# Kernel tuning notes

Measured on AMD Instinct MI355X. Metric: run time of the kernel, lower is better.

Reference implementation:

```python
import jax, jax.numpy as jnp
import numpy as np

L, D, H, F = 6, 768, 12, 3072   # layers, d_model, heads, mlp hidden
B, S = 2, 2048                   # batch, seq_len
DH = D // H                      # head dim
EPS = 1e-5


def _layer_norm(x, w, b):
    mu = jnp.mean(x, axis=-1, keepdims=True)
    var = jnp.mean(jnp.square(x - mu), axis=-1, keepdims=True)
    return (x - mu) * jax.lax.rsqrt(var + EPS) * w + b


def setup_inputs() -> dict:
    key = jax.random.key(0)
    ks = jax.random.split(key, 8)
    w = lambda k, shape: jax.random.normal(k, shape, dtype=jnp.float32) * 0.02
    return {
        "x": jax.random.normal(ks[0], (B, S, D), dtype=jnp.float32),
        # attention projections, stacked over layers; weights stored (d_in, d_out)
        "Wq": w(ks[1], (L, D, D)), "bq": jnp.zeros((L, D), jnp.float32),
        "Wk": w(ks[2], (L, D, D)), "bk": jnp.zeros((L, D), jnp.float32),
        "Wv": w(ks[3], (L, D, D)), "bv": jnp.zeros((L, D), jnp.float32),
        "Wo": w(ks[4], (L, D, D)), "bo": jnp.zeros((L, D), jnp.float32),
        "ln1_w": jnp.ones((L, D), jnp.float32), "ln1_b": jnp.zeros((L, D), jnp.float32),
        "W1": w(ks[5], (L, D, F)), "b1": jnp.zeros((L, F), jnp.float32),
        "W2": w(ks[6], (L, F, D)), "b2": jnp.zeros((L, D), jnp.float32),
        "ln2_w": jnp.ones((L, D), jnp.float32), "ln2_b": jnp.zeros((L, D), jnp.float32),
        "lnf_w": jnp.ones((D,), jnp.float32), "lnf_b": jnp.zeros((D,), jnp.float32),
    }


def reference(x, Wq, bq, Wk, bk, Wv, bv, Wo, bo, ln1_w, ln1_b,
              W1, b1, W2, b2, ln2_w, ln2_b, lnf_w, lnf_b):
    scale = DH ** (-0.5)
    for i in range(L):
        # pre-norm MSA block; NB: residual uses the normalized x, as in source
        xn = _layer_norm(x, ln1_w[i], ln1_b[i])
        q = (xn @ Wq[i] + bq[i]).reshape(B, S, H, DH).transpose(0, 2, 1, 3)
        k = (xn @ Wk[i] + bk[i]).reshape(B, S, H, DH).transpose(0, 2, 1, 3)
        v = (xn @ Wv[i] + bv[i]).reshape(B, S, H, DH).transpose(0, 2, 1, 3)
        att = jax.nn.softmax(scale * jnp.einsum('bhqd,bhkd->bhqk', q, k), axis=-1)
        out = jnp.einsum('bhqk,bhkd->bhqd', att, v)
        out = out.transpose(0, 2, 1, 3).reshape(B, S, D)
        x = xn + (out @ Wo[i] + bo[i])
        # pre-norm FFN block; residual uses the normalized x, as in source
        xn2 = _layer_norm(x, ln2_w[i], ln2_b[i])
        h = jax.nn.gelu(xn2 @ W1[i] + b1[i], approximate=False)
        x = xn2 + (h @ W2[i] + b2[i])
    return _layer_norm(x, lnf_w, lnf_b)
```

## Files before the change

### kernel.cpp

```cpp
#include <hip/hip_runtime.h>
#include <stdint.h>

typedef unsigned short u16;
typedef unsigned int   u32;

#define L_N  6
#define D_N  768
#define F_N  3072
#define H_N  12
#define B_N  2
#define S_N  2048
#define BS_N 4096
#define QKV_N 2304
#define CSC  0.18033688011112042f
#define DTHR 11.54f

using bf16x8 = __attribute__((ext_vector_type(8))) short;
using f32x4  = __attribute__((ext_vector_type(4))) float;
using f32x16 = __attribute__((ext_vector_type(16))) float;
using u32x2  = __attribute__((ext_vector_type(2))) unsigned int;

__device__ __forceinline__ u16 f2bf(float f) {
  u32 x = __builtin_bit_cast(u32, f);
  x += 0x7FFFu + ((x >> 16) & 1u);
  return (u16)(x >> 16);
}

__device__ __forceinline__ float bf2f(u16 v) {
  return __builtin_bit_cast(float, (u32)v << 16);
}

__device__ __forceinline__ u32 cvt_pk_bf16(float lo, float hi) {
  u32 r;
  asm("v_cvt_pk_bf16_f32 %0, %1, %2" : "=v"(r) : "v"(lo), "v"(hi));
  return r;
}

#define GLOAD16(g, l)                                                                     \
  __builtin_amdgcn_global_load_lds((const __attribute__((address_space(1))) void*)(g),    \
                                   (__attribute__((address_space(3))) void*)(l), 16, 0, 0)

__global__ __launch_bounds__(256) void transpose_cast_kernel(
    const float* __restrict__ in, u16* __restrict__ out, int K, int N,
    size_t out_lstride, int out_rowoff)
{
  __shared__ float tile[32][33];
  const int l  = blockIdx.z;
  const int n0 = blockIdx.x * 32, k0 = blockIdx.y * 32;
  const int tx = threadIdx.x & 31, ty = threadIdx.x >> 5;
  const float* src = in + (size_t)l * K * N;
  u16* dst = out + (size_t)l * out_lstride + (size_t)out_rowoff * K;
#pragma unroll
  for (int i = 0; i < 4; ++i)
    tile[ty + i * 8][tx] = src[(size_t)(k0 + ty + i * 8) * N + n0 + tx];
  __syncthreads();
#pragma unroll
  for (int i = 0; i < 4; ++i)
    dst[(size_t)(n0 + ty + i * 8) * K + k0 + tx] = f2bf(tile[tx][ty + i * 8]);
}

__global__ __launch_bounds__(256) void concat_bias_kernel(
    const float* __restrict__ bq, const float* __restrict__ bk,
    const float* __restrict__ bv, float* __restrict__ out)
{
  const int i = blockIdx.x * 256 + threadIdx.x;
  const int l = i / QKV_N, c = i - l * QKV_N;
  float v = (c < 768) ? bq[l * 768 + c]
          : (c < 1536) ? bk[l * 768 + c - 768]
                       : bv[l * 768 + c - 1536];
  out[i] = v;
}

template<bool BF16IN>
__global__ __launch_bounds__(256) void ln_kernel(
    const void* __restrict__ xv, const float* __restrict__ w, const float* __restrict__ b,
    float* __restrict__ outF, u16* __restrict__ outB)
{
  const int row = blockIdx.x, tid = threadIdx.x;
  float v[3];
  float s = 0.f;
  if (BF16IN) {
    const u16* xr = (const u16*)xv + (size_t)row * D_N;
#pragma unroll
    for (int i = 0; i < 3; ++i) { v[i] = bf2f(xr[tid + i * 256]); s += v[i]; }
  } else {
    const float* xr = (const float*)xv + (size_t)row * D_N;
#pragma unroll
    for (int i = 0; i < 3; ++i) { v[i] = xr[tid + i * 256]; s += v[i]; }
  }
  __shared__ float red[8];
  const int wave = tid >> 6, lane = tid & 63;
#pragma unroll
  for (int o = 32; o > 0; o >>= 1) s += __shfl_down(s, o, 64);
  if (lane == 0) red[wave] = s;
  __syncthreads();
  const float mu = (red[0] + red[1] + red[2] + red[3]) * (1.f / D_N);
  float d2 = 0.f;
#pragma unroll
  for (int i = 0; i < 3; ++i) { float d = v[i] - mu; d2 += d * d; }
#pragma unroll
  for (int o = 32; o > 0; o >>= 1) d2 += __shfl_down(d2, o, 64);
  if (lane == 0) red[4 + wave] = d2;
  __syncthreads();
  const float var = (red[4] + red[5] + red[6] + red[7]) * (1.f / D_N);
  const float rs = rsqrtf(var + 1e-5f);
#pragma unroll
  for (int i = 0; i < 3; ++i) {
    const int c = tid + i * 256;
    const float o = (v[i] - mu) * rs * w[c] + b[c];
    if (outF) outF[(size_t)row * D_N + c] = o;
    if (outB) outB[(size_t)row * D_N + c] = f2bf(o);
  }
}

template<bool GELU, bool OUTB, bool SCALEQ>
__global__ __launch_bounds__(256) void gemm_kernel(
    const u16* __restrict__ A, const u16* __restrict__ Wt,
    const float* __restrict__ bias,
    u16* __restrict__ outB, int M, int N, int K)
{
  __shared__ __align__(16) u16 As[2][128 * 32];
  __shared__ __align__(16) u16 Bs[2][128 * 32];
  const int tid  = threadIdx.x;
  const int wave = tid >> 6, lane = tid & 63;
  const int lr = lane & 15, lg = lane >> 4;
  const int row0 = blockIdx.x * 128, col0 = blockIdx.y * 128;
  const int wr = (wave >> 1) * 64, wc = (wave & 1) * 64;

  const int cb0 = wave * 64;
  const int cb1 = 256 + wave * 64;
  const int r0s = (cb0 + lane) >> 2, c0s = ((cb0 + lane) & 3) << 3;
  const int r1s = (cb1 + lane) >> 2, c1s = ((cb1 + lane) & 3) << 3;

  f32x4 acc[4][4] = {};

#define STAGE(cbuf, kk)                                                           \
  do {                                                                            \
    GLOAD16(A  + (size_t)(row0 + r0s) * K + (kk) + c0s, &As[cbuf][cb0 * 8]);      \
    GLOAD16(Wt + (size_t)(col0 + r0s) * K + (kk) + c0s, &Bs[cbuf][cb0 * 8]);      \
    GLOAD16(A  + (size_t)(row0 + r1s) * K + (kk) + c1s, &As[cbuf][cb1 * 8]);      \
    GLOAD16(Wt + (size_t)(col0 + r1s) * K + (kk) + c1s, &Bs[cbuf][cb1 * 8]);      \
  } while (0)

  STAGE(0, 0);
  __syncthreads();

  int c = 0;
  for (int k0 = 0; k0 < K; k0 += 32, c ^= 1) {
    if (k0 + 32 < K) STAGE(c ^ 1, k0 + 32);
    bf16x8 af[4], bfr[4];
#pragma unroll
    for (int m = 0; m < 4; ++m)
      af[m] = *(const bf16x8*)&As[c][(wr + m * 16 + lr) * 32 + lg * 8];
#pragma unroll
    for (int n = 0; n < 4; ++n)
      bfr[n] = *(const bf16x8*)&Bs[c][(wc + n * 16 + lr) * 32 + lg * 8];
    __builtin_amdgcn_s_setprio(1);
#pragma unroll
    for (int m = 0; m < 4; ++m)
#pragma unroll
      for (int n = 0; n < 4; ++n)
        acc[m][n] = __builtin_amdgcn_mfma_f32_16x16x32_bf16(af[m], bfr[n], acc[m][n], 0, 0, 0);
    __builtin_amdgcn_s_setprio(0);
    __syncthreads();
  }
#undef STAGE

#pragma unroll
  for (int m = 0; m < 4; ++m)
#pragma unroll
    for (int n = 0; n < 4; ++n) {
      const int col = col0 + wc + n * 16 + lr;
      const float bv = bias[col];
#pragma unroll
      for (int r = 0; r < 4; ++r) {
        const int row = row0 + wr + m * 16 + lg * 4 + r;
        float v = acc[m][n][r] + bv;
        if (GELU) v = 0.5f * v * (1.f + erff(v * 0.70710678118f));
        if (SCALEQ && col < 768) v *= CSC;
        const size_t idx = (size_t)row * N + col;
        if (OUTB) outB[idx] = f2bf(v);
      }
    }
}

__global__ __launch_bounds__(256) void gemm64_kernel(
    const u16* __restrict__ A, const u16* __restrict__ Wt,
    const float* __restrict__ bias, const u16* __restrict__ resid,
    u16* __restrict__ outB, int M, int N, int K)
{
  __shared__ __align__(16) u16 As[2][64 * 32];
  __shared__ __align__(16) u16 Bs[2][64 * 32];
  const int tid  = threadIdx.x;
  const int wave = tid >> 6, lane = tid & 63;
  const int lr = lane & 15, lg = lane >> 4;
  const int row0 = blockIdx.x * 64, col0 = blockIdx.y * 64;
  const int wr = (wave >> 1) * 32, wc = (wave & 1) * 32;

  const int cb = wave * 64;
  const int ch = cb + lane;
  const int rs = ch >> 2, cs = (ch & 3) << 3;

  f32x4 acc[2][2] = {};

#define STAGE64(cbuf, kk)                                                         \
  do {                                                                            \
    GLOAD16(A  + (size_t)(row0 + rs) * K + (kk) + cs, &As[cbuf][cb * 8]);         \
    GLOAD16(Wt + (size_t)(col0 + rs) * K + (kk) + cs, &Bs[cbuf][cb * 8]);         \
  } while (0)

  STAGE64(0, 0);
  __syncthreads();

  int c = 0;
  for (int k0 = 0; k0 < K; k0 += 32, c ^= 1) {
    if (k0 + 32 < K) STAGE64(c ^ 1, k0 + 32);
    bf16x8 af[2], bfr[2];
#pragma unroll
    for (int m = 0; m < 2; ++m)
      af[m] = *(const bf16x8*)&As[c][(wr + m * 16 + lr) * 32 + lg * 8];
#pragma unroll
    for (int n = 0; n < 2; ++n)
      bfr[n] = *(const bf16x8*)&Bs[c][(wc + n * 16 + lr) * 32 + lg * 8];
    __builtin_amdgcn_s_setprio(1);
#pragma unroll
    for (int m = 0; m < 2; ++m)
#pragma unroll
      for (int n = 0; n < 2; ++n)
        acc[m][n] = __builtin_amdgcn_mfma_f32_16x16x32_bf16(af[m], bfr[n], acc[m][n], 0, 0, 0);
    __builtin_amdgcn_s_setprio(0);
    __syncthreads();
  }
#undef STAGE64

#pragma unroll
  for (int m = 0; m < 2; ++m)
#pragma unroll
    for (int n = 0; n < 2; ++n) {
      const int col = col0 + wc + n * 16 + lr;
      const float bv = bias[col];
#pragma unroll
      for (int r = 0; r < 4; ++r) {
        const int row = row0 + wr + m * 16 + lg * 4 + r;
        const size_t idx = (size_t)row * N + col;
        outB[idx] = f2bf(acc[m][n][r] + bv + bf2f(resid[idx]));
      }
    }
}

__global__ __launch_bounds__(256) void attn_kernel(
    const u16* __restrict__ QKV, u16* __restrict__ O)
{
  constexpr int LDQ = QKV_N;
  constexpr int NT  = S_N / 64;
  __shared__ __align__(16) u16 Ks [64 * 72];
  __shared__ __align__(16) u16 VTs[64 * 72];
  const int tid  = threadIdx.x;
  const int wave = tid >> 6, lane = tid & 63;
  const int l31 = lane & 31, l5 = lane >> 5;
  const int bh = blockIdx.y;
  const int b = bh / H_N, h = bh - b * H_N;
  const int q0 = blockIdx.x * 128;
  const size_t rowbase = (size_t)b * S_N * LDQ;
  const u16* Qg = QKV + rowbase + h * 64;
  const u16* Kg = QKV + rowbase + 768 + h * 64;
  const u16* Vg = QKV + rowbase + 1536 + h * 64;

  const int qrow = q0 + wave * 32 + l31;
  bf16x8 qf[4];
#pragma unroll
  for (int ks = 0; ks < 4; ++ks)
    qf[ks] = *(const bf16x8*)(Qg + (size_t)qrow * LDQ + ks * 16 + l5 * 8);

  f32x16 o0 = {}, o1 = {};
  float m = -1e30f, l = 0.f;

  const int kr = tid >> 2, kc = (tid & 3) * 16;
  const int pp = tid >> 3, cg = tid & 7;

  const u16* gk0 = Kg + (size_t)kr * LDQ + kc;
  const u16* gv0 = Vg + (size_t)(2 * pp) * LDQ + cg * 8;
  uint4 nk0 = *(const uint4*)gk0, nk1 = *(const uint4*)(gk0 + 8);
  uint4 nv0 = *(const uint4*)gv0, nv1 = *(const uint4*)(gv0 + LDQ);

  for (int t = 0; t < NT; ++t) {
    __syncthreads();
    {
      *(uint4*)&Ks[kr * 72 + kc]     = nk0;
      *(uint4*)&Ks[kr * 72 + kc + 8] = nk1;
      const u16* a0 = (const u16*)&nv0;
      const u16* a1 = (const u16*)&nv1;
#pragma unroll
      for (int j = 0; j < 8; ++j) {
        const int jj = (j + cg) & 7;
        *(u32*)&VTs[(cg * 8 + jj) * 72 + 2 * pp] = (u32)a0[jj] | ((u32)a1[jj] << 16);
      }
    }
    __syncthreads();

    if (t + 1 < NT) {
      const u16* gk1 = Kg + (size_t)((t + 1) * 64 + kr) * LDQ + kc;
      const u16* gv1 = Vg + (size_t)((t + 1) * 64 + 2 * pp) * LDQ + cg * 8;
      nk0 = *(const uint4*)gk1; nk1 = *(const uint4*)(gk1 + 8);
      nv0 = *(const uint4*)gv1; nv1 = *(const uint4*)(gv1 + LDQ);
    }

    f32x16 sv0 = {}, sv1 = {};
    __builtin_amdgcn_s_setprio(1);
#pragma unroll
    for (int ks = 0; ks < 4; ++ks) {
      const bf16x8 kf0 = *(const bf16x8*)&Ks[(l31)      * 72 + ks * 16 + l5 * 8];
      const bf16x8 kf1 = *(const bf16x8*)&Ks[(32 + l31) * 72 + ks * 16 + l5 * 8];
      sv0 = __builtin_amdgcn_mfma_f32_32x32x16_bf16(kf0, qf[ks], sv0, 0, 0, 0);
      sv1 = __builtin_amdgcn_mfma_f32_32x32x16_bf16(kf1, qf[ks], sv1, 0, 0, 0);
    }
    __builtin_amdgcn_s_setprio(0);

    float mx = sv0[0];
#pragma unroll
    for (int i = 0; i < 16; ++i) mx = fmaxf(mx, sv0[i]);
#pragma unroll
    for (int i = 0; i < 16; ++i) mx = fmaxf(mx, sv1[i]);
    {
      const u32 mb = __builtin_bit_cast(u32, mx);
      const u32x2 rr = __builtin_amdgcn_permlane32_swap(mb, mb, false, false);
      mx = fmaxf(__builtin_bit_cast(float, rr[0]), __builtin_bit_cast(float, rr[1]));
    }
    if (!__all(mx - m <= DTHR)) {
      const float mn = fmaxf(m, mx);
      const float al = __builtin_amdgcn_exp2f(m - mn);
      m = mn;
      l *= al;
#pragma unroll
      for (int i = 0; i < 16; ++i) { o0[i] *= al; o1[i] *= al; }
    }
    float rs = 0.f;
#pragma unroll
    for (int i = 0; i < 16; ++i) {
      const float e = __builtin_amdgcn_exp2f(sv0[i] - m);
      sv0[i] = e; rs += e;
    }
#pragma unroll
    for (int i = 0; i < 16; ++i) {
      const float e = __builtin_amdgcn_exp2f(sv1[i] - m);
      sv1[i] = e; rs += e;
    }
    {
      const u32 sb = __builtin_bit_cast(u32, rs);
      const u32x2 rr = __builtin_amdgcn_permlane32_swap(sb, sb, false, false);
      rs = __builtin_bit_cast(float, rr[0]) + __builtin_bit_cast(float, rr[1]);
    }
    l += rs;

    bf16x8 pb[4];
#pragma unroll
    for (int kb = 0; kb < 2; ++kb) {
      const f32x16& p = kb ? sv1 : sv0;
#pragma unroll
      for (int half = 0; half < 2; ++half) {
        const int o8 = half * 8;
        const u32 a0 = cvt_pk_bf16(p[o8 + 0], p[o8 + 1]);
        const u32 b0 = cvt_pk_bf16(p[o8 + 4], p[o8 + 5]);
        const u32 a1 = cvt_pk_bf16(p[o8 + 2], p[o8 + 3]);
        const u32 b1 = cvt_pk_bf16(p[o8 + 6], p[o8 + 7]);
        const u32x2 r0 = __builtin_amdgcn_permlane32_swap(a0, b0, false, false);
        const u32x2 r1 = __builtin_amdgcn_permlane32_swap(a1, b1, false, false);
        u32 w[4] = { r0[0], r1[0], r0[1], r1[1] };
        pb[kb * 2 + half] = __builtin_bit_cast(bf16x8, *(const uint4*)w);
      }
    }

    __builtin_amdgcn_s_setprio(1);
#pragma unroll
    for (int ks2 = 0; ks2 < 4; ++ks2) {
      const bf16x8 vf0 = *(const bf16x8*)&VTs[(l31)      * 72 + ks2 * 16 + l5 * 8];
      const bf16x8 vf1 = *(const bf16x8*)&VTs[(32 + l31) * 72 + ks2 * 16 + l5 * 8];
      o0 = __builtin_amdgcn_mfma_f32_32x32x16_bf16(vf0, pb[ks2], o0, 0, 0, 0);
      o1 = __builtin_amdgcn_mfma_f32_32x32x16_bf16(vf1, pb[ks2], o1, 0, 0, 0);
    }
    __builtin_amdgcn_s_setprio(0);
  }

  const float inv = 1.f / l;
  u16* orow = O + (size_t)(b * S_N + qrow) * D_N + h * 64;
#pragma unroll
  for (int r = 0; r < 16; r += 2) {
    const int dh = (r & 3) + 8 * (r >> 2) + 4 * l5;
    *(u32*)(orow + dh)      = cvt_pk_bf16(o0[r] * inv, o0[r + 1] * inv);
    *(u32*)(orow + dh + 32) = cvt_pk_bf16(o1[r] * inv, o1[r + 1] * inv);
  }
}

extern "C" void kernel_launch(void* const* d_in, const int* in_sizes, int n_in,
                              void* d_out, int out_size, void* d_ws, size_t ws_size,
                              hipStream_t stream)
{
  (void)in_sizes; (void)n_in; (void)out_size; (void)ws_size;
  const float* x0   = (const float*)d_in[0];
  const float* Wq   = (const float*)d_in[1];
  const float* bq   = (const float*)d_in[2];
  const float* Wk   = (const float*)d_in[3];
  const float* bk   = (const float*)d_in[4];
  const float* Wv   = (const float*)d_in[5];
  const float* bv   = (const float*)d_in[6];
  const float* Wo   = (const float*)d_in[7];
  const float* bo   = (const float*)d_in[8];
  const float* ln1w = (const float*)d_in[9];
  const float* ln1b = (const float*)d_in[10];
  const float* W1   = (const float*)d_in[11];
  const float* b1   = (const float*)d_in[12];
  const float* W2   = (const float*)d_in[13];
  const float* b2   = (const float*)d_in[14];
  const float* ln2w = (const float*)d_in[15];
  const float* ln2b = (const float*)d_in[16];
  const float* lnfw = (const float*)d_in[17];
  const float* lnfb = (const float*)d_in[18];

  char* ws = (char*)d_ws;
  size_t off = 0;
  auto alloc = [&](size_t bytes) {
    char* p = ws + off; off += (bytes + 255) & ~(size_t)255; return p;
  };
  u16*   wqkv_t = (u16*)alloc((size_t)L_N * QKV_N * D_N * 2);
  u16*   wo_t   = (u16*)alloc((size_t)L_N * D_N * D_N * 2);
  u16*   w1_t   = (u16*)alloc((size_t)L_N * D_N * F_N * 2);
  u16*   w2_t   = (u16*)alloc((size_t)L_N * D_N * F_N * 2);
  float* bqkv   = (float*)alloc((size_t)L_N * QKV_N * 4);
  u16*   x_b    = (u16*)alloc((size_t)BS_N * D_N * 2);
  u16*   xn_b   = (u16*)alloc((size_t)BS_N * D_N * 2);
  u16*   qkvb   = (u16*)alloc((size_t)BS_N * QKV_N * 2);
  u16*   ab     = (u16*)alloc((size_t)BS_N * D_N * 2);
  u16*   hb     = (u16*)alloc((size_t)BS_N * F_N * 2);

  const size_t dd = (size_t)D_N * D_N, qs = (size_t)QKV_N * D_N, df = (size_t)D_N * F_N;
  transpose_cast_kernel<<<dim3(D_N/32, D_N/32, L_N), 256, 0, stream>>>(Wq, wqkv_t, D_N, D_N, qs, 0);
  transpose_cast_kernel<<<dim3(D_N/32, D_N/32, L_N), 256, 0, stream>>>(Wk, wqkv_t, D_N, D_N, qs, 768);
  transpose_cast_kernel<<<dim3(D_N/32, D_N/32, L_N), 256, 0, stream>>>(Wv, wqkv_t, D_N, D_N, qs, 1536);
  transpose_cast_kernel<<<dim3(D_N/32, D_N/32, L_N), 256, 0, stream>>>(Wo, wo_t, D_N, D_N, dd, 0);
  transpose_cast_kernel<<<dim3(F_N/32, D_N/32, L_N), 256, 0, stream>>>(W1, w1_t, D_N, F_N, df, 0);
  transpose_cast_kernel<<<dim3(D_N/32, F_N/32, L_N), 256, 0, stream>>>(W2, w2_t, F_N, D_N, df, 0);
  concat_bias_kernel<<<(L_N * QKV_N) / 256, 256, 0, stream>>>(bq, bk, bv, bqkv);

  const dim3 gQKV(BS_N / 128, QKV_N / 128);
  const dim3 gF  (BS_N / 128, F_N / 128);
  const dim3 g64 (BS_N / 64,  D_N / 64);
  const dim3 gA  (S_N / 128, B_N * H_N);

  for (int i = 0; i < L_N; ++i) {
    if (i == 0)
      ln_kernel<false><<<BS_N, 256, 0, stream>>>(x0, ln1w, ln1b, nullptr, xn_b);
    else
      ln_kernel<true><<<BS_N, 256, 0, stream>>>(x_b, ln1w + i * D_N, ln1b + i * D_N, nullptr, xn_b);
    gemm_kernel<false,true,true><<<gQKV, 256, 0, stream>>>(
        xn_b, wqkv_t + (size_t)i * qs, bqkv + (size_t)i * QKV_N, qkvb, BS_N, QKV_N, D_N);
    attn_kernel<<<gA, 256, 0, stream>>>(qkvb, ab);
    gemm64_kernel<<<g64, 256, 0, stream>>>(
        ab, wo_t + (size_t)i * dd, bo + i * D_N, xn_b, x_b, BS_N, D_N, D_N);
    ln_kernel<true><<<BS_N, 256, 0, stream>>>(x_b, ln2w + i * D_N, ln2b + i * D_N, nullptr, xn_b);
    gemm_kernel<true,true,false><<<gF, 256, 0, stream>>>(
        xn_b, w1_t + (size_t)i * df, b1 + i * F_N, hb, BS_N, F_N, D_N);
    gemm64_kernel<<<g64, 256, 0, stream>>>(
        hb, w2_t + (size_t)i * df, b2 + i * D_N, xn_b, x_b, BS_N, D_N, F_N);
  }
  ln_kernel<true><<<BS_N, 256, 0, stream>>>(x_b, lnfw, lnfb, (float*)d_out, nullptr);
}
```

Measured before the change: 1.371 ms.

## Split attention KV range across two blocks and combine partials

Attention now splits the key/value sequence into two halves along a new grid dimension. Each block writes unnormalized fp32 partial outputs plus its running max and sum, and a new combine kernel merges the halves with a log-sum-exp rescale. This doubles the number of attention blocks to improve GPU occupancy and wave balance. In exchange it adds fp32 partial-result traffic through the reused FFN hidden buffer and one extra kernel launch per layer.

```diff
diff --git a/kernel.cpp b/kernel.cpp
--- a/kernel.cpp
+++ b/kernel.cpp
@@ -249,7 +249,7 @@
 }
 
 __global__ __launch_bounds__(256) void attn_kernel(
-    const u16* __restrict__ QKV, u16* __restrict__ O)
+    const u16* __restrict__ QKV, float* __restrict__ Opart, float* __restrict__ Ml)
 {
   constexpr int LDQ = QKV_N;
   constexpr int NT  = S_N / 64;
@@ -261,6 +261,8 @@
   const int bh = blockIdx.y;
   const int b = bh / H_N, h = bh - b * H_N;
   const int q0 = blockIdx.x * 128;
+  const int z  = blockIdx.z;
+  const int t0 = z * (NT / 2), t1 = (z + 1) * (NT / 2);
   const size_t rowbase = (size_t)b * S_N * LDQ;
   const u16* Qg = QKV + rowbase + h * 64;
   const u16* Kg = QKV + rowbase + 768 + h * 64;
@@ -278,12 +280,12 @@
   const int kr = tid >> 2, kc = (tid & 3) * 16;
   const int pp = tid >> 3, cg = tid & 7;
 
-  const u16* gk0 = Kg + (size_t)kr * LDQ + kc;
-  const u16* gv0 = Vg + (size_t)(2 * pp) * LDQ + cg * 8;
+  const u16* gk0 = Kg + (size_t)(t0 * 64 + kr) * LDQ + kc;
+  const u16* gv0 = Vg + (size_t)(t0 * 64 + 2 * pp) * LDQ + cg * 8;
   uint4 nk0 = *(const uint4*)gk0, nk1 = *(const uint4*)(gk0 + 8);
   uint4 nv0 = *(const uint4*)gv0, nv1 = *(const uint4*)(gv0 + LDQ);
 
-  for (int t = 0; t < NT; ++t) {
+  for (int t = t0; t < t1; ++t) {
     __syncthreads();
     {
       *(uint4*)&Ks[kr * 72 + kc]     = nk0;
@@ -298,7 +300,7 @@
     }
     __syncthreads();
 
-    if (t + 1 < NT) {
+    if (t + 1 < t1) {
       const u16* gk1 = Kg + (size_t)((t + 1) * 64 + kr) * LDQ + kc;
       const u16* gv1 = Vg + (size_t)((t + 1) * 64 + 2 * pp) * LDQ + cg * 8;
       nk0 = *(const uint4*)gk1; nk1 = *(const uint4*)(gk1 + 8);
@@ -381,14 +383,38 @@
     __builtin_amdgcn_s_setprio(0);
   }
 
-  const float inv = 1.f / l;
-  u16* orow = O + (size_t)(b * S_N + qrow) * D_N + h * 64;
+  float* op = Opart + (((size_t)z * B_N * H_N + bh) * S_N + qrow) * 64;
 #pragma unroll
   for (int r = 0; r < 16; r += 2) {
     const int dh = (r & 3) + 8 * (r >> 2) + 4 * l5;
-    *(u32*)(orow + dh)      = cvt_pk_bf16(o0[r] * inv, o0[r + 1] * inv);
-    *(u32*)(orow + dh + 32) = cvt_pk_bf16(o1[r] * inv, o1[r + 1] * inv);
-  }
+    *(float2*)(op + dh)      = float2{o0[r], o0[r + 1]};
+    *(float2*)(op + dh + 32) = float2{o1[r], o1[r + 1]};
+  }
+  if (l5 == 0) {
+    float* mlp = Ml + (((size_t)z * B_N * H_N + bh) * S_N + qrow) * 2;
+    mlp[0] = m; mlp[1] = l;
+  }
+}
+
+__global__ __launch_bounds__(256) void attn_combine_kernel(
+    const float* __restrict__ Opart, const float* __restrict__ Ml, u16* __restrict__ O)
+{
+  constexpr size_t HALF = (size_t)B_N * H_N * S_N;
+  const int tid = threadIdx.x;
+  const int lane = tid & 63, grp = tid >> 6;
+  const size_t row = (size_t)blockIdx.x * 4 + grp;
+  const float* p0 = Opart + row * 64;
+  const float* p1 = p0 + HALF * 64;
+  const float m0 = Ml[row * 2], l0 = Ml[row * 2 + 1];
+  const float m1 = Ml[(row + HALF) * 2], l1 = Ml[(row + HALF) * 2 + 1];
+  const float mm = fmaxf(m0, m1);
+  const float a0 = __builtin_amdgcn_exp2f(m0 - mm);
+  const float a1 = __builtin_amdgcn_exp2f(m1 - mm);
+  const float inv = 1.f / (a0 * l0 + a1 * l1);
+  const float o = (a0 * p0[lane] + a1 * p1[lane]) * inv;
+  const int bh = (int)(row / S_N), s = (int)(row % S_N);
+  const int b = bh / H_N, h = bh - b * H_N;
+  O[((size_t)b * S_N + s) * D_N + h * 64 + lane] = f2bf(o);
 }
 
 extern "C" void kernel_launch(void* const* d_in, const int* in_sizes, int n_in,
@@ -431,6 +457,8 @@
   u16*   qkvb   = (u16*)alloc((size_t)BS_N * QKV_N * 2);
   u16*   ab     = (u16*)alloc((size_t)BS_N * D_N * 2);
   u16*   hb     = (u16*)alloc((size_t)BS_N * F_N * 2);
+  float* ml     = (float*)alloc((size_t)2 * B_N * H_N * S_N * 2 * 4);
+  float* opart  = (float*)hb;
 
   const size_t dd = (size_t)D_N * D_N, qs = (size_t)QKV_N * D_N, df = (size_t)D_N * F_N;
   transpose_cast_kernel<<<dim3(D_N/32, D_N/32, L_N), 256, 0, stream>>>(Wq, wqkv_t, D_N, D_N, qs, 0);
@@ -444,7 +472,7 @@
   const dim3 gQKV(BS_N / 128, QKV_N / 128);
   const dim3 gF  (BS_N / 128, F_N / 128);
   const dim3 g64 (BS_N / 64,  D_N / 64);
-  const dim3 gA  (S_N / 128, B_N * H_N);
+  const dim3 gA  (S_N / 128, B_N * H_N, 2);
 
   for (int i = 0; i < L_N; ++i) {
     if (i == 0)
@@ -453,7 +481,8 @@
       ln_kernel<true><<<BS_N, 256, 0, stream>>>(x_b, ln1w + i * D_N, ln1b + i * D_N, nullptr, xn_b);
     gemm_kernel<false,true,true><<<gQKV, 256, 0, stream>>>(
         xn_b, wqkv_t + (size_t)i * qs, bqkv + (size_t)i * QKV_N, qkvb, BS_N, QKV_N, D_N);
-    attn_kernel<<<gA, 256, 0, stream>>>(qkvb, ab);
+    attn_kernel<<<gA, 256, 0, stream>>>(qkvb, opart, ml);
+    attn_combine_kernel<<<(B_N * H_N * S_N) / 4, 256, 0, stream>>>(opart, ml, ab);
     gemm64_kernel<<<g64, 256, 0, stream>>>(
         ab, wo_t + (size_t)i * dd, bo + i * D_N, xn_b, x_b, BS_N, D_N, D_N);
     ln_kernel<true><<<BS_N, 256, 0, stream>>>(x_b, ln2w + i * D_N, ln2b + i * D_N, nullptr, xn_b);
```

New measurement: 1.334 ms. 1.03x faster.
